# Performance work log

Hardware: AMD Instinct MI355X
Metric: run time of the kernel (lower is better)

Reference implementation:

```python
import jax, jax.numpy as jnp
import numpy as np
from jax import lax

HEADS = 8
DIM_HEAD = 64
INNER = HEADS * DIM_HEAD  # 512
LOG_SCALE_MAX = float(np.log(100.0))  # clamp for clamp_exp (SwinV2-style max temperature 1/0.01)
EPS_NORM = 1e-12  # F.normalize eps
EPS_LN = 1e-5


def setup_inputs() -> dict:
    key = jax.random.key(0)
    ks = jax.random.split(key, 6)
    b, c, h, w = 2, 256, 48, 48
    x = jax.random.normal(ks[0], (b, c, h, w), jnp.float32)
    w_in = jax.random.normal(ks[1], (3 * INNER, c), jnp.float32) * (c ** -0.5)
    b_in = jnp.zeros((3 * INNER,), jnp.float32)
    # learnable log-scale, init log(d_head ** -0.5), per head
    softmax_scale = jnp.full((HEADS, 1, 1), float(np.log(DIM_HEAD ** -0.5)), jnp.float32)
    w_dw = jax.random.normal(ks[2], (INNER, 1, 3, 3), jnp.float32) * (1.0 / 3.0)
    w_pw = jax.random.normal(ks[3], (2 * c, INNER), jnp.float32) * (INNER ** -0.5)
    gamma = jnp.full((2 * c,), 1e-3, jnp.float32)  # norm init_weight=0.001
    beta = jnp.zeros((2 * c,), jnp.float32)
    return {"x": x, "w_in": w_in, "b_in": b_in, "softmax_scale": softmax_scale,
            "w_dw": w_dw, "w_pw": w_pw, "gamma": gamma, "beta": beta}


def _l2norm(t):
    n = jnp.sqrt(jnp.sum(t * t, axis=-1, keepdims=True))
    return t / jnp.maximum(n, EPS_NORM)


def reference(x, w_in, b_in, softmax_scale, w_dw, w_pw, gamma, beta):
    b, c, h, w = x.shape
    s = h * w
    # proj_in: 1x1 conv then 'b (h c) x y -> b h x y c'
    y = jnp.einsum('bchw,oc->bohw', x, w_in) + b_in[None, :, None, None]
    y = y.reshape(b, HEADS, 3 * DIM_HEAD, h, w).transpose(0, 1, 3, 4, 2)  # b H x y (3*dh)
    y = y.reshape(b, HEADS, s, 3 * DIM_HEAD)
    q, k, v = jnp.split(y, 3, axis=-1)  # each [b, H, s, dh]
    # scaled cosine attention
    qn, kn = _l2norm(q), _l2norm(k)
    scale = jnp.exp(jnp.minimum(softmax_scale, LOG_SCALE_MAX))  # clamp_exp, [H,1,1]
    sim = jnp.einsum('bhid,bhjd->bhij', qn, kn) * scale[None]
    attn = jax.nn.softmax(sim, axis=-1)
    out = jnp.einsum('bhij,bhjd->bhid', attn, v)  # [b,H,s,dh]
    # unsplit heads -> 'b (h w) c' -> 'b c h w'
    update = out.transpose(0, 2, 1, 3).reshape(b, s, INNER)
    update = update.transpose(0, 2, 1).reshape(b, INNER, h, w)
    # proj_out: depthwise 3x3 (no bias) + pointwise 1x1 (no bias)
    dw = lax.conv_general_dilated(update, w_dw, (1, 1), 'SAME',
                                  feature_group_count=INNER,
                                  dimension_numbers=('NCHW', 'OIHW', 'NCHW'))
    pw = jnp.einsum('bchw,oc->bohw', dw, w_pw)  # [b, 2c, h, w]
    # channelwise layernorm with small init weight (norm_scales_and_shifts)
    mu = jnp.mean(pw, axis=1, keepdims=True)
    var = jnp.var(pw, axis=1, keepdims=True)
    normed = (pw - mu) * lax.rsqrt(var + EPS_LN)
    normed = normed * gamma[None, :, None, None] + beta[None, :, None, None]
    scales, shifts = jnp.split(normed, 2, axis=1)  # each [b, c, h, w]
    return shifts + x * scales
```

## Files before the change

kernel.cpp:

```cpp
#include <hip/hip_runtime.h>

#define B_ 2
#define C_ 256
#define S_ 2304
#define DH_ 64
#define O3_ 1536
#define INNER_ 512
#define LOGSMAX 4.605170185988092f
#define LOG2E 1.4426950408889634f

typedef __attribute__((ext_vector_type(8))) short short8;
typedef __attribute__((ext_vector_type(4))) float f32x4;
typedef __attribute__((ext_vector_type(16))) float f32x16;
typedef __attribute__((ext_vector_type(4))) unsigned short us4;
typedef __bf16 bf16x8 __attribute__((ext_vector_type(8)));

__device__ __forceinline__ unsigned short f2bf(float f) {
  unsigned u = __builtin_bit_cast(unsigned, f);
  u += 0x7FFFu + ((u >> 16) & 1u);
  return (unsigned short)(u >> 16);
}
__device__ __forceinline__ float bf2f(unsigned short h) {
  return __builtin_bit_cast(float, (unsigned)h << 16);
}
__device__ __forceinline__ bf16x8 as_bf(short8 v) {
  return __builtin_bit_cast(bf16x8, v);
}
__device__ __forceinline__ float fexp2(float x) {
#if __has_builtin(__builtin_amdgcn_exp2f)
  return __builtin_amdgcn_exp2f(x);
#else
  return __expf(x * 0.6931471805599453f);
#endif
}
__device__ __forceinline__ float frcp(float x) {
#if __has_builtin(__builtin_amdgcn_rcpf)
  return __builtin_amdgcn_rcpf(x);
#else
  return 1.f / x;
#endif
}

__global__ __launch_bounds__(256) void k_prep(const float* __restrict__ x,
                                              const float* __restrict__ w_in,
                                              const float* __restrict__ w_pw,
                                              unsigned short* __restrict__ xT,
                                              unsigned short* __restrict__ w_inb,
                                              unsigned short* __restrict__ w_pwb) {
  __shared__ float tile[64][65];
  int blk = blockIdx.x;
  int t = threadIdx.x;
  if (blk < 288) {
    int p0 = (blk % 36) * 64, c0 = ((blk / 36) % 4) * 64, b = blk / 144;
    const float* xb = x + (size_t)b * C_ * S_;
#pragma unroll
    for (int i = 0; i < 16; i++) {
      int c = i * 4 + (t >> 6);
      int p = t & 63;
      tile[c][p] = xb[(size_t)(c0 + c) * S_ + p0 + p];
    }
    __syncthreads();
    unsigned short* xTb = xT + (size_t)b * S_ * C_;
#pragma unroll
    for (int i = 0; i < 16; i++) {
      int p = i * 4 + (t >> 6);
      int c = t & 63;
      xTb[(size_t)(p0 + p) * C_ + c0 + c] = f2bf(tile[c][p]);
    }
  } else if (blk < 288 + 1536) {
    int i = (blk - 288) * 256 + t;
    w_inb[i] = f2bf(w_in[i]);
  } else {
    int i = (blk - 1824) * 256 + t;
    w_pwb[i] = f2bf(w_pw[i]);
  }
}

__global__ __launch_bounds__(256) void k_gemm(const unsigned short* __restrict__ A,
                                              const unsigned short* __restrict__ BT,
                                              void* __restrict__ outp,
                                              int M, int N, int K, int bf16out) {
  __shared__ __align__(16) unsigned short As[128][72];
  __shared__ __align__(16) unsigned short Bs[128][72];
  int t = threadIdx.x;
  int lane = t & 63, wv = t >> 6;
  int quad = lane >> 4, r15 = lane & 15;
  int wm = wv >> 1, wn = wv & 1;
  int m0 = blockIdx.y * 128, n0 = blockIdx.x * 128;
  int b = blockIdx.z;
  const unsigned short* BTb = BT + (size_t)b * N * K;

  f32x4 acc[4][4] = {};

  int srow = t >> 2;
  int sc = (t & 3) * 16;
  const unsigned short* ag = A + (size_t)(m0 + srow) * K + sc;
  const unsigned short* bg = BTb + (size_t)(n0 + srow) * K + sc;

  for (int k0 = 0; k0 < K; k0 += 64) {
    short8 a00 = *(const short8*)(ag + k0);
    short8 a01 = *(const short8*)(ag + k0 + 8);
    short8 a10 = *(const short8*)(ag + (size_t)64 * K + k0);
    short8 a11 = *(const short8*)(ag + (size_t)64 * K + k0 + 8);
    short8 b00 = *(const short8*)(bg + k0);
    short8 b01 = *(const short8*)(bg + k0 + 8);
    short8 b10 = *(const short8*)(bg + (size_t)64 * K + k0);
    short8 b11 = *(const short8*)(bg + (size_t)64 * K + k0 + 8);
    __syncthreads();
    *(short8*)&As[srow][sc] = a00;
    *(short8*)&As[srow][sc + 8] = a01;
    *(short8*)&As[srow + 64][sc] = a10;
    *(short8*)&As[srow + 64][sc + 8] = a11;
    *(short8*)&Bs[srow][sc] = b00;
    *(short8*)&Bs[srow][sc + 8] = b01;
    *(short8*)&Bs[srow + 64][sc] = b10;
    *(short8*)&Bs[srow + 64][sc + 8] = b11;
    __syncthreads();
#pragma unroll
    for (int ks = 0; ks < 2; ks++) {
      short8 af[4], bfr[4];
#pragma unroll
      for (int i = 0; i < 4; i++) af[i] = *(const short8*)&As[wm * 64 + i * 16 + r15][ks * 32 + quad * 8];
#pragma unroll
      for (int j = 0; j < 4; j++) bfr[j] = *(const short8*)&Bs[wn * 64 + j * 16 + r15][ks * 32 + quad * 8];
#pragma unroll
      for (int i = 0; i < 4; i++)
#pragma unroll
        for (int j = 0; j < 4; j++)
          acc[i][j] = __builtin_amdgcn_mfma_f32_16x16x32_bf16(as_bf(af[i]), as_bf(bfr[j]), acc[i][j], 0, 0, 0);
    }
  }
  if (bf16out) {
    unsigned short* Cb = (unsigned short*)outp + (size_t)b * M * N;
#pragma unroll
    for (int i = 0; i < 4; i++)
#pragma unroll
      for (int j = 0; j < 4; j++)
#pragma unroll
        for (int rr = 0; rr < 4; rr++) {
          int row = m0 + wm * 64 + i * 16 + quad * 4 + rr;
          int col = n0 + wn * 64 + j * 16 + r15;
          Cb[(size_t)row * N + col] = f2bf(acc[i][j][rr]);
        }
  } else {
    float* Cb = (float*)outp + (size_t)b * M * N;
#pragma unroll
    for (int i = 0; i < 4; i++)
#pragma unroll
      for (int j = 0; j < 4; j++)
#pragma unroll
        for (int rr = 0; rr < 4; rr++) {
          int row = m0 + wm * 64 + i * 16 + quad * 4 + rr;
          int col = n0 + wn * 64 + j * 16 + r15;
          Cb[(size_t)row * N + col] = acc[i][j][rr];
        }
  }
}

__global__ __launch_bounds__(192) void k_norm_qkv(const unsigned short* __restrict__ y,
                                                  const float* __restrict__ b_in,
                                                  const float* __restrict__ ss,
                                                  unsigned short* __restrict__ qn,
                                                  unsigned short* __restrict__ kn,
                                                  unsigned short* __restrict__ vT) {
  int t = threadIdx.x;
  int seg = t >> 6;
  int p = blockIdx.x * 64 + (t & 63);
  int bh = blockIdx.y;
  int b = bh >> 3, h = bh & 7;
  int obase = h * 192 + seg * 64;
  const unsigned short* yb = y + ((size_t)b * O3_ + obase) * S_ + p;
  const float* bb = b_in + obase;
  if (seg < 2) {
    float scale = (seg == 0) ? __expf(fminf(ss[h], LOGSMAX)) * LOG2E : 1.f;
    unsigned packed[32];
    float sumsq = 0.f;
#pragma unroll
    for (int d = 0; d < 64; d += 2) {
      float v0 = bf2f(yb[(size_t)d * S_]) + bb[d];
      float v1 = bf2f(yb[(size_t)(d + 1) * S_]) + bb[d + 1];
      sumsq += v0 * v0 + v1 * v1;
      packed[d >> 1] = (unsigned)f2bf(v0) | ((unsigned)f2bf(v1) << 16);
    }
    float inv = scale / fmaxf(sqrtf(sumsq), 1e-12f);
    unsigned short* dst = (seg == 0 ? qn : kn) + ((size_t)bh * S_ + p) * 64;
    unsigned outw[32];
#pragma unroll
    for (int i = 0; i < 32; i++) {
      float v0 = bf2f((unsigned short)(packed[i] & 0xffffu)) * inv;
      float v1 = bf2f((unsigned short)(packed[i] >> 16)) * inv;
      outw[i] = (unsigned)f2bf(v0) | ((unsigned)f2bf(v1) << 16);
    }
    uint4* d4 = (uint4*)dst;
#pragma unroll
    for (int i = 0; i < 8; i++)
      d4[i] = make_uint4(outw[4 * i], outw[4 * i + 1], outw[4 * i + 2], outw[4 * i + 3]);
  } else {
#pragma unroll
    for (int d = 0; d < 64; d++) {
      float v = bf2f(yb[(size_t)d * S_]) + bb[d];
      vT[((size_t)bh * DH_ + d) * S_ + p] = f2bf(v);
    }
  }
}

__global__ __launch_bounds__(128) void k_attn(const unsigned short* __restrict__ qn,
                                              const unsigned short* __restrict__ kn,
                                              const unsigned short* __restrict__ vT,
                                              const float* __restrict__ ss,
                                              unsigned short* __restrict__ attnp,
                                              float* __restrict__ lp) {
  __shared__ __align__(16) unsigned short Ks[64][72];
  __shared__ __align__(16) unsigned short Vs[64][72];
  __shared__ __align__(16) unsigned short Ps[2][32][72];
  int t = threadIdx.x;
  int w = t >> 6;
  int lane = t & 63;
  int l31 = lane & 31, hi = lane >> 5;
  int bh = blockIdx.x;
  int q0 = blockIdx.y * 64 + w * 32;
  int split = blockIdx.z;
  int ktbase = split * 18;
  const unsigned short* qb = qn + (size_t)bh * S_ * DH_;
  const unsigned short* kb = kn + (size_t)bh * S_ * DH_;
  const unsigned short* vb = vT + (size_t)bh * DH_ * S_;
  float shift2 = __expf(fminf(ss[bh & 7], LOGSMAX)) * LOG2E;

  const unsigned short* qrow = qb + (size_t)(q0 + l31) * DH_ + hi * 8;
  short8 qf[4];
#pragma unroll
  for (int ks = 0; ks < 4; ks++) qf[ks] = *(const short8*)(qrow + ks * 16);

  const f32x16 z16 = {};
  f32x16 O0 = z16, O1 = z16;
  float l_part = 0.f;

  int row = t >> 1;
  int c0 = (t & 1) * 32;
  const unsigned short* kg = kb + (size_t)row * DH_ + c0;
  const unsigned short* vg = vb + (size_t)row * S_ + c0;

  short8 kr[4], vr[4];
#pragma unroll
  for (int j = 0; j < 4; j++) {
    kr[j] = *(const short8*)(kg + (size_t)ktbase * 64 * DH_ + j * 8);
    vr[j] = *(const short8*)(vg + ktbase * 64 + j * 8);
  }

  for (int i = 0; i < 18; i++) {
    __syncthreads();
#pragma unroll
    for (int j = 0; j < 4; j++) {
      *(short8*)&Ks[row][c0 + j * 8] = kr[j];
      *(short8*)&Vs[row][c0 + j * 8] = vr[j];
    }
    __syncthreads();
    if (i < 17) {
      int kt = ktbase + i + 1;
#pragma unroll
      for (int j = 0; j < 4; j++) {
        kr[j] = *(const short8*)(kg + (size_t)kt * 64 * DH_ + j * 8);
        vr[j] = *(const short8*)(vg + kt * 64 + j * 8);
      }
    }
    f32x16 sc0, sc1;
    {
      short8 a0 = *(const short8*)&Ks[l31][hi * 8];
      short8 a1 = *(const short8*)&Ks[32 + l31][hi * 8];
      sc0 = __builtin_amdgcn_mfma_f32_32x32x16_bf16(as_bf(a0), as_bf(qf[0]), z16, 0, 0, 0);
      sc1 = __builtin_amdgcn_mfma_f32_32x32x16_bf16(as_bf(a1), as_bf(qf[0]), z16, 0, 0, 0);
    }
#pragma unroll
    for (int ks = 1; ks < 4; ks++) {
      short8 a0 = *(const short8*)&Ks[l31][ks * 16 + hi * 8];
      short8 a1 = *(const short8*)&Ks[32 + l31][ks * 16 + hi * 8];
      sc0 = __builtin_amdgcn_mfma_f32_32x32x16_bf16(as_bf(a0), as_bf(qf[ks]), sc0, 0, 0, 0);
      sc1 = __builtin_amdgcn_mfma_f32_32x32x16_bf16(as_bf(a1), as_bf(qf[ks]), sc1, 0, 0, 0);
    }
    float lsum = 0.f;
#pragma unroll
    for (int mt = 0; mt < 2; mt++) {
      const f32x16& s = mt ? sc1 : sc0;
#pragma unroll
      for (int g = 0; g < 4; g++) {
        float e0 = fexp2(s[g * 4 + 0] - shift2);
        float e1 = fexp2(s[g * 4 + 1] - shift2);
        float e2 = fexp2(s[g * 4 + 2] - shift2);
        float e3 = fexp2(s[g * 4 + 3] - shift2);
        lsum += (e0 + e1) + (e2 + e3);
        us4 pk = {f2bf(e0), f2bf(e1), f2bf(e2), f2bf(e3)};
        *(us4*)&Ps[w][l31][mt * 32 + g * 8 + hi * 4] = pk;
      }
    }
    l_part += lsum;
#pragma unroll
    for (int ks = 0; ks < 4; ks++) {
      short8 pb = *(const short8*)&Ps[w][l31][ks * 16 + hi * 8];
      short8 va0 = *(const short8*)&Vs[l31][ks * 16 + hi * 8];
      short8 va1 = *(const short8*)&Vs[32 + l31][ks * 16 + hi * 8];
      O0 = __builtin_amdgcn_mfma_f32_32x32x16_bf16(as_bf(va0), as_bf(pb), O0, 0, 0, 0);
      O1 = __builtin_amdgcn_mfma_f32_32x32x16_bf16(as_bf(va1), as_bf(pb), O1, 0, 0, 0);
    }
  }
  float l = l_part + __shfl_xor(l_part, 32);
  if (hi == 0) lp[((size_t)(split * 16 + bh)) * S_ + q0 + l31] = l;
  unsigned short* orow = attnp + (((size_t)(split * 16 + bh)) * S_ + q0 + l31) * DH_;
#pragma unroll
  for (int mt = 0; mt < 2; mt++) {
    const f32x16& O = mt ? O1 : O0;
#pragma unroll
    for (int g = 0; g < 4; g++) {
      us4 o4 = {f2bf(O[g * 4 + 0]), f2bf(O[g * 4 + 1]), f2bf(O[g * 4 + 2]), f2bf(O[g * 4 + 3])};
      *(us4*)&orow[mt * 32 + g * 8 + hi * 4] = o4;
    }
  }
}

__global__ __launch_bounds__(256) void k_dwconv(const unsigned short* __restrict__ attnp,
                                                const float* __restrict__ lp,
                                                const float* __restrict__ w_dw,
                                                unsigned short* __restrict__ dwb) {
  int t = threadIdx.x;
  int d = t & 63;
  int pj = t >> 6;
  int p = blockIdx.x * 4 + pj;
  int bh = blockIdx.y;
  int b = bh >> 3, h = bh & 7;
  int yy = p / 48, xx = p % 48;
  const unsigned short* a0 = attnp + (size_t)bh * S_ * DH_ + d;
  const unsigned short* a1 = attnp + ((size_t)(16 + bh)) * S_ * DH_ + d;
  const float* l0 = lp + (size_t)bh * S_;
  const float* l1 = lp + (size_t)(16 + bh) * S_;
  int ch = h * 64 + d;
  float w[9];
#pragma unroll
  for (int i = 0; i < 9; i++) w[i] = w_dw[ch * 9 + i];
  float acc = 0.f;
#pragma unroll
  for (int dy = -1; dy <= 1; dy++) {
    int y2 = yy + dy;
    if (y2 < 0 || y2 >= 48) continue;
#pragma unroll
    for (int dx = -1; dx <= 1; dx++) {
      int x2 = xx + dx;
      if (x2 < 0 || x2 >= 48) continue;
      int p2 = y2 * 48 + x2;
      float rl = frcp(l0[p2] + l1[p2]);
      float v = (bf2f(a0[(size_t)p2 * DH_]) + bf2f(a1[(size_t)p2 * DH_])) * rl;
      acc += v * w[(dy + 1) * 3 + dx + 1];
    }
  }
  dwb[((size_t)b * S_ + p) * INNER_ + ch] = f2bf(acc);
}

__global__ __launch_bounds__(256) void k_ln_final(const float* __restrict__ pw,
                                                  const float* __restrict__ gamma,
                                                  const float* __restrict__ beta,
                                                  const float* __restrict__ x,
                                                  float* __restrict__ out) {
  __shared__ float s_sum[16][17];
  __shared__ float s_ss[16][17];
  int t = threadIdx.x;
  int pl = t & 15, cq = t >> 4;
  int gid = blockIdx.x;
  int b = gid / (S_ / 16);
  int p = (gid % (S_ / 16)) * 16 + pl;
  const float* pwb = pw + (size_t)b * INNER_ * S_;
  float sum = 0.f, sq = 0.f;
#pragma unroll
  for (int j = 0; j < 32; j++) {
    float v = pwb[(size_t)(cq * 32 + j) * S_ + p];
    sum += v;
    sq += v * v;
  }
  s_sum[cq][pl] = sum;
  s_ss[cq][pl] = sq;
  __syncthreads();
  float tot = 0.f, tss = 0.f;
#pragma unroll
  for (int i = 0; i < 16; i++) {
    tot += s_sum[i][pl];
    tss += s_ss[i][pl];
  }
  float mu = tot * (1.f / 512.f);
  float var = tss * (1.f / 512.f) - mu * mu;
  float rsig = rsqrtf(var + 1e-5f);
  const float* xb = x + (size_t)b * C_ * S_;
  float* ob = out + (size_t)b * C_ * S_;
#pragma unroll
  for (int j = 0; j < 16; j++) {
    int cc = cq * 16 + j;
    float scv = (pwb[(size_t)cc * S_ + p] - mu) * rsig * gamma[cc] + beta[cc];
    float shv = (pwb[(size_t)(cc + 256) * S_ + p] - mu) * rsig * gamma[cc + 256] + beta[cc + 256];
    ob[(size_t)cc * S_ + p] = shv + xb[(size_t)cc * S_ + p] * scv;
  }
}

extern "C" void kernel_launch(void* const* d_in, const int* in_sizes, int n_in,
                              void* d_out, int out_size, void* d_ws, size_t ws_size,
                              hipStream_t stream) {
  const float* x = (const float*)d_in[0];
  const float* w_in = (const float*)d_in[1];
  const float* b_in = (const float*)d_in[2];
  const float* ss = (const float*)d_in[3];
  const float* w_dw = (const float*)d_in[4];
  const float* w_pw = (const float*)d_in[5];
  const float* gamma = (const float*)d_in[6];
  const float* beta = (const float*)d_in[7];
  float* out = (float*)d_out;
  char* ws = (char*)d_ws;

  unsigned short* xT = (unsigned short*)(ws + 0);
  unsigned short* w_inb = (unsigned short*)(ws + 2359296);
  unsigned short* w_pwb = (unsigned short*)(ws + 3145728);
  unsigned short* qn = (unsigned short*)(ws + 3670016);
  unsigned short* kn = (unsigned short*)(ws + 8388608);
  unsigned short* vT = (unsigned short*)(ws + 13107200);
  unsigned short* dwb = (unsigned short*)(ws + 17825792);
  float* lp = (float*)(ws + 22544384);
  char* big = ws + 22839296;
  unsigned short* y = (unsigned short*)big;
  float* pw = (float*)big;
  unsigned short* attnp = (unsigned short*)(ws + 36995072);

  k_prep<<<2848, 256, 0, stream>>>(x, w_in, w_pw, xT, w_inb, w_pwb);
  k_gemm<<<dim3(18, 12, 2), 256, 0, stream>>>(w_inb, xT, y, O3_, S_, C_, 1);
  k_norm_qkv<<<dim3(36, 16), 192, 0, stream>>>(y, b_in, ss, qn, kn, vT);
  k_attn<<<dim3(16, 36, 2), 128, 0, stream>>>(qn, kn, vT, ss, attnp, lp);
  k_dwconv<<<dim3(576, 16), 256, 0, stream>>>(attnp, lp, w_dw, dwb);
  k_gemm<<<dim3(18, 4, 2), 256, 0, stream>>>(w_pwb, dwb, pw, INNER_, S_, INNER_, 0);
  k_ln_final<<<288, 256, 0, stream>>>(pw, gamma, beta, x, out);
}
```

Measured before the change: 180.9 us.

## Load K/V fragments directly from global in attention; shrink GEMM M-tile to 64

The attention kernel no longer stages K and V tiles through shared memory with block barriers. Each wave now loads its MFMA operand fragments for K and V straight from global memory (relying on L2/L1 reuse across the two waves), and the P scratch padding changes to 76. This removes the two __syncthreads per iteration and the LDS round trip, at the cost of duplicated global loads and no explicit prefetch. Separately, the GEMM tile goes from 128x128 to 64x128 with each wave owning a 64x32 slab, doubling the grid to improve occupancy and wave count on the small GEMMs.

Result: slower. 220.2 us (+21.7%).

```diff
diff --git a/kernel.cpp b/kernel.cpp
--- a/kernel.cpp
+++ b/kernel.cpp
@@ -80,53 +80,48 @@
                                               const unsigned short* __restrict__ BT,
                                               void* __restrict__ outp,
                                               int M, int N, int K, int bf16out) {
-  __shared__ __align__(16) unsigned short As[128][72];
+  __shared__ __align__(16) unsigned short As[64][72];
   __shared__ __align__(16) unsigned short Bs[128][72];
   int t = threadIdx.x;
   int lane = t & 63, wv = t >> 6;
   int quad = lane >> 4, r15 = lane & 15;
-  int wm = wv >> 1, wn = wv & 1;
-  int m0 = blockIdx.y * 128, n0 = blockIdx.x * 128;
+  int m0 = blockIdx.y * 64, n0 = blockIdx.x * 128;
   int b = blockIdx.z;
   const unsigned short* BTb = BT + (size_t)b * N * K;
 
-  f32x4 acc[4][4] = {};
-
-  int srow = t >> 2;
-  int sc = (t & 3) * 16;
-  const unsigned short* ag = A + (size_t)(m0 + srow) * K + sc;
-  const unsigned short* bg = BTb + (size_t)(n0 + srow) * K + sc;
+  f32x4 acc[4][2] = {};
+
+  int srA = t >> 2, scA = (t & 3) * 16;
+  int srB = t >> 1, scB = (t & 1) * 32;
+  const unsigned short* ag = A + (size_t)(m0 + srA) * K + scA;
+  const unsigned short* bg = BTb + (size_t)(n0 + srB) * K + scB;
 
   for (int k0 = 0; k0 < K; k0 += 64) {
-    short8 a00 = *(const short8*)(ag + k0);
-    short8 a01 = *(const short8*)(ag + k0 + 8);
-    short8 a10 = *(const short8*)(ag + (size_t)64 * K + k0);
-    short8 a11 = *(const short8*)(ag + (size_t)64 * K + k0 + 8);
-    short8 b00 = *(const short8*)(bg + k0);
-    short8 b01 = *(const short8*)(bg + k0 + 8);
-    short8 b10 = *(const short8*)(bg + (size_t)64 * K + k0);
-    short8 b11 = *(const short8*)(bg + (size_t)64 * K + k0 + 8);
+    short8 a0 = *(const short8*)(ag + k0);
+    short8 a1 = *(const short8*)(ag + k0 + 8);
+    short8 b0 = *(const short8*)(bg + k0);
+    short8 b1 = *(const short8*)(bg + k0 + 8);
+    short8 b2 = *(const short8*)(bg + k0 + 16);
+    short8 b3 = *(const short8*)(bg + k0 + 24);
     __syncthreads();
-    *(short8*)&As[srow][sc] = a00;
-    *(short8*)&As[srow][sc + 8] = a01;
-    *(short8*)&As[srow + 64][sc] = a10;
-    *(short8*)&As[srow + 64][sc + 8] = a11;
-    *(short8*)&Bs[srow][sc] = b00;
-    *(short8*)&Bs[srow][sc + 8] = b01;
-    *(short8*)&Bs[srow + 64][sc] = b10;
-    *(short8*)&Bs[srow + 64][sc + 8] = b11;
+    *(short8*)&As[srA][scA] = a0;
+    *(short8*)&As[srA][scA + 8] = a1;
+    *(short8*)&Bs[srB][scB] = b0;
+    *(short8*)&Bs[srB][scB + 8] = b1;
+    *(short8*)&Bs[srB][scB + 16] = b2;
+    *(short8*)&Bs[srB][scB + 24] = b3;
     __syncthreads();
 #pragma unroll
     for (int ks = 0; ks < 2; ks++) {
-      short8 af[4], bfr[4];
-#pragma unroll
-      for (int i = 0; i < 4; i++) af[i] = *(const short8*)&As[wm * 64 + i * 16 + r15][ks * 32 + quad * 8];
-#pragma unroll
-      for (int j = 0; j < 4; j++) bfr[j] = *(const short8*)&Bs[wn * 64 + j * 16 + r15][ks * 32 + quad * 8];
+      short8 af[4], bfr[2];
+#pragma unroll
+      for (int i = 0; i < 4; i++) af[i] = *(const short8*)&As[i * 16 + r15][ks * 32 + quad * 8];
+#pragma unroll
+      for (int j = 0; j < 2; j++) bfr[j] = *(const short8*)&Bs[wv * 32 + j * 16 + r15][ks * 32 + quad * 8];
 #pragma unroll
       for (int i = 0; i < 4; i++)
 #pragma unroll
-        for (int j = 0; j < 4; j++)
+        for (int j = 0; j < 2; j++)
           acc[i][j] = __builtin_amdgcn_mfma_f32_16x16x32_bf16(as_bf(af[i]), as_bf(bfr[j]), acc[i][j], 0, 0, 0);
     }
   }
@@ -135,11 +130,11 @@
 #pragma unroll
     for (int i = 0; i < 4; i++)
 #pragma unroll
-      for (int j = 0; j < 4; j++)
+      for (int j = 0; j < 2; j++)
 #pragma unroll
         for (int rr = 0; rr < 4; rr++) {
-          int row = m0 + wm * 64 + i * 16 + quad * 4 + rr;
-          int col = n0 + wn * 64 + j * 16 + r15;
+          int row = m0 + i * 16 + quad * 4 + rr;
+          int col = n0 + wv * 32 + j * 16 + r15;
           Cb[(size_t)row * N + col] = f2bf(acc[i][j][rr]);
         }
   } else {
@@ -147,11 +142,11 @@
 #pragma unroll
     for (int i = 0; i < 4; i++)
 #pragma unroll
-      for (int j = 0; j < 4; j++)
+      for (int j = 0; j < 2; j++)
 #pragma unroll
         for (int rr = 0; rr < 4; rr++) {
-          int row = m0 + wm * 64 + i * 16 + quad * 4 + rr;
-          int col = n0 + wn * 64 + j * 16 + r15;
+          int row = m0 + i * 16 + quad * 4 + rr;
+          int col = n0 + wv * 32 + j * 16 + r15;
           Cb[(size_t)row * N + col] = acc[i][j][rr];
         }
   }
@@ -210,9 +205,7 @@
                                               const float* __restrict__ ss,
                                               unsigned short* __restrict__ attnp,
                                               float* __restrict__ lp) {
-  __shared__ __align__(16) unsigned short Ks[64][72];
-  __shared__ __align__(16) unsigned short Vs[64][72];
-  __shared__ __align__(16) unsigned short Ps[2][32][72];
+  __shared__ __align__(16) unsigned short Ps[2][32][76];
   int t = threadIdx.x;
   int w = t >> 6;
   int lane = t & 63;
@@ -235,47 +228,33 @@
   f32x16 O0 = z16, O1 = z16;
   float l_part = 0.f;
 
-  int row = t >> 1;
-  int c0 = (t & 1) * 32;
-  const unsigned short* kg = kb + (size_t)row * DH_ + c0;
-  const unsigned short* vg = vb + (size_t)row * S_ + c0;
-
-  short8 kr[4], vr[4];
-#pragma unroll
-  for (int j = 0; j < 4; j++) {
-    kr[j] = *(const short8*)(kg + (size_t)ktbase * 64 * DH_ + j * 8);
-    vr[j] = *(const short8*)(vg + ktbase * 64 + j * 8);
-  }
+  const unsigned short* kg0 = kb + ((size_t)(ktbase * 64) + l31) * DH_ + hi * 8;
+  const unsigned short* kg1 = kg0 + (size_t)32 * DH_;
+  const unsigned short* vg0 = vb + (size_t)l31 * S_ + ktbase * 64 + hi * 8;
+  const unsigned short* vg1 = vg0 + (size_t)32 * S_;
 
   for (int i = 0; i < 18; i++) {
-    __syncthreads();
-#pragma unroll
-    for (int j = 0; j < 4; j++) {
-      *(short8*)&Ks[row][c0 + j * 8] = kr[j];
-      *(short8*)&Vs[row][c0 + j * 8] = vr[j];
-    }
-    __syncthreads();
-    if (i < 17) {
-      int kt = ktbase + i + 1;
-#pragma unroll
-      for (int j = 0; j < 4; j++) {
-        kr[j] = *(const short8*)(kg + (size_t)kt * 64 * DH_ + j * 8);
-        vr[j] = *(const short8*)(vg + kt * 64 + j * 8);
-      }
+    size_t koff = (size_t)i * 64 * DH_;
+    int voff = i * 64;
+    short8 ka[4], kc[4];
+#pragma unroll
+    for (int ks = 0; ks < 4; ks++) {
+      ka[ks] = *(const short8*)(kg0 + koff + ks * 16);
+      kc[ks] = *(const short8*)(kg1 + koff + ks * 16);
+    }
+    short8 va[4], vc[4];
+#pragma unroll
+    for (int ks = 0; ks < 4; ks++) {
+      va[ks] = *(const short8*)(vg0 + voff + ks * 16);
+      vc[ks] = *(const short8*)(vg1 + voff + ks * 16);
     }
     f32x16 sc0, sc1;
-    {
-      short8 a0 = *(const short8*)&Ks[l31][hi * 8];
-      short8 a1 = *(const short8*)&Ks[32 + l31][hi * 8];
-      sc0 = __builtin_amdgcn_mfma_f32_32x32x16_bf16(as_bf(a0), as_bf(qf[0]), z16, 0, 0, 0);
-      sc1 = __builtin_amdgcn_mfma_f32_32x32x16_bf16(as_bf(a1), as_bf(qf[0]), z16, 0, 0, 0);
-    }
+    sc0 = __builtin_amdgcn_mfma_f32_32x32x16_bf16(as_bf(ka[0]), as_bf(qf[0]), z16, 0, 0, 0);
+    sc1 = __builtin_amdgcn_mfma_f32_32x32x16_bf16(as_bf(kc[0]), as_bf(qf[0]), z16, 0, 0, 0);
 #pragma unroll
     for (int ks = 1; ks < 4; ks++) {
-      short8 a0 = *(const short8*)&Ks[l31][ks * 16 + hi * 8];
-      short8 a1 = *(const short8*)&Ks[32 + l31][ks * 16 + hi * 8];
-      sc0 = __builtin_amdgcn_mfma_f32_32x32x16_bf16(as_bf(a0), as_bf(qf[ks]), sc0, 0, 0, 0);
-      sc1 = __builtin_amdgcn_mfma_f32_32x32x16_bf16(as_bf(a1), as_bf(qf[ks]), sc1, 0, 0, 0);
+      sc0 = __builtin_amdgcn_mfma_f32_32x32x16_bf16(as_bf(ka[ks]), as_bf(qf[ks]), sc0, 0, 0, 0);
+      sc1 = __builtin_amdgcn_mfma_f32_32x32x16_bf16(as_bf(kc[ks]), as_bf(qf[ks]), sc1, 0, 0, 0);
     }
     float lsum = 0.f;
 #pragma unroll
@@ -296,10 +275,8 @@
 #pragma unroll
     for (int ks = 0; ks < 4; ks++) {
       short8 pb = *(const short8*)&Ps[w][l31][ks * 16 + hi * 8];
-      short8 va0 = *(const short8*)&Vs[l31][ks * 16 + hi * 8];
-      short8 va1 = *(const short8*)&Vs[32 + l31][ks * 16 + hi * 8];
-      O0 = __builtin_amdgcn_mfma_f32_32x32x16_bf16(as_bf(va0), as_bf(pb), O0, 0, 0, 0);
-      O1 = __builtin_amdgcn_mfma_f32_32x32x16_bf16(as_bf(va1), as_bf(pb), O1, 0, 0, 0);
+      O0 = __builtin_amdgcn_mfma_f32_32x32x16_bf16(as_bf(va[ks]), as_bf(pb), O0, 0, 0, 0);
+      O1 = __builtin_amdgcn_mfma_f32_32x32x16_bf16(as_bf(vc[ks]), as_bf(pb), O1, 0, 0, 0);
     }
   }
   float l = l_part + __shfl_xor(l_part, 32);
@@ -424,10 +401,10 @@
   unsigned short* attnp = (unsigned short*)(ws + 36995072);
 
   k_prep<<<2848, 256, 0, stream>>>(x, w_in, w_pw, xT, w_inb, w_pwb);
-  k_gemm<<<dim3(18, 12, 2), 256, 0, stream>>>(w_inb, xT, y, O3_, S_, C_, 1);
+  k_gemm<<<dim3(18, 24, 2), 256, 0, stream>>>(w_inb, xT, y, O3_, S_, C_, 1);
   k_norm_qkv<<<dim3(36, 16), 192, 0, stream>>>(y, b_in, ss, qn, kn, vT);
   k_attn<<<dim3(16, 36, 2), 128, 0, stream>>>(qn, kn, vT, ss, attnp, lp);
   k_dwconv<<<dim3(576, 16), 256, 0, stream>>>(attnp, lp, w_dw, dwb);
-  k_gemm<<<dim3(18, 4, 2), 256, 0, stream>>>(w_pwb, dwb, pw, INNER_, S_, INNER_, 0);
+  k_gemm<<<dim3(18, 8, 2), 256, 0, stream>>>(w_pwb, dwb, pw, INNER_, S_, INNER_, 0);
   k_ln_final<<<288, 256, 0, stream>>>(pw, gamma, beta, x, out);
 }
```
